# Kernel tuning notes

Hardware: AMD Instinct MI355X
Metric: run time of the kernel (lower is better)

## Reference

```python
import jax, jax.numpy as jnp
import numpy as np

T, B, I, H, O, L = 512, 64, 256, 1024, 256, 3


def _gru_layer(x_seq, h0, w_ih, w_hh, b_ih, b_hh):
    """PyTorch-style GRU layer. x_seq: [T,B,Iin], h0: [B,H].
    Gate order in stacked weights is (r, z, n), matching torch.nn.GRU."""
    # Precompute all input-side gate projections with one big GEMM: [T,B,3H]
    gi = jnp.einsum('tbi,gi->tbg', x_seq, w_ih) + b_ih

    def step(h, gi_t):
        gh = h @ w_hh.T + b_hh                      # [B,3H]
        i_r, i_z, i_n = jnp.split(gi_t, 3, axis=-1)
        h_r, h_z, h_n = jnp.split(gh, 3, axis=-1)
        r = jax.nn.sigmoid(i_r + h_r)
        z = jax.nn.sigmoid(i_z + h_z)
        n = jnp.tanh(i_n + r * h_n)
        h_new = (1.0 - z) * n + z * h
        return h_new, h_new

    h_last, ys = jax.lax.scan(step, h0, gi)
    return ys, h_last


def setup_inputs() -> dict:
    key = jax.random.key(0)
    ks = jax.random.split(key, 16)
    s = 1.0 / np.sqrt(H)  # torch init scale ~ U(-1/sqrt(H), 1/sqrt(H))
    inp = {
        'x': jax.random.normal(ks[0], (T, B, I), jnp.float32),
        'h0': jax.random.normal(ks[1], (L, B, H), jnp.float32),
        'fc_w': jax.random.uniform(ks[2], (O, H), jnp.float32, -s, s),
        'fc_b': jax.random.uniform(ks[3], (O,), jnp.float32, -s, s),
    }
    k_idx = 4
    for l in range(L):
        iin = I if l == 0 else H
        inp[f'w_ih_l{l}'] = jax.random.uniform(ks[k_idx], (3 * H, iin), jnp.float32, -s, s)
        inp[f'w_hh_l{l}'] = jax.random.uniform(ks[k_idx + 1], (3 * H, H), jnp.float32, -s, s)
        inp[f'b_ih_l{l}'] = jax.random.uniform(ks[k_idx + 2], (3 * H,), jnp.float32, -s, s)
        inp[f'b_hh_l{l}'] = jax.random.uniform(ks[k_idx + 3], (3 * H,), jnp.float32, -s, s)
        k_idx += 4
    return inp


def reference(x, h0,
              w_ih_l0, w_hh_l0, b_ih_l0, b_hh_l0,
              w_ih_l1, w_hh_l1, b_ih_l1, b_hh_l1,
              w_ih_l2, w_hh_l2, b_ih_l2, b_hh_l2,
              fc_w, fc_b):
    layer_params = [
        (w_ih_l0, w_hh_l0, b_ih_l0, b_hh_l0),
        (w_ih_l1, w_hh_l1, b_ih_l1, b_hh_l1),
        (w_ih_l2, w_hh_l2, b_ih_l2, b_hh_l2),
    ]
    out = x
    h_lasts = []
    for l, (wi, wh, bi, bh) in enumerate(layer_params):
        out, h_l = _gru_layer(out, h0[l], wi, wh, bi, bh)
        h_lasts.append(h_l)
    y = out @ fc_w.T + fc_b        # [T,B,O]
    h_final = jnp.stack(h_lasts)   # [L,B,H]
    return y, h_final
```

## Files before the change

### kernel.cpp

```cpp
#include <hip/hip_runtime.h>
#include <cstdint>
#include <cstddef>

#define TT 512
#define BB 64
#define II 256
#define HH 1024
#define OO 256
#define LL 3
#define NBLK 192
#define TSLOTS 513
#define DD 2
#define SSTEPS (TT + 2*DD + 1)
#define LDS_GI   98304
#define GI_STRIDE 68
#define LDS_HT   (98304 + 26112)
#define LDS_TOTAL (LDS_HT + 2048)

typedef _Float16 half8 __attribute__((ext_vector_type(8)));
typedef float floatx4 __attribute__((ext_vector_type(4)));
typedef float float4v __attribute__((ext_vector_type(4)));

__device__ __forceinline__ floatx4 mfma16(half8 a, half8 b, floatx4 c) {
    return __builtin_amdgcn_mfma_f32_16x16x32_f16(a, b, c, 0, 0, 0);
}

__device__ __forceinline__ half8 ld_f32x8_cvt(const float* p) {
    float4v a = *(const float4v*)p;
    float4v b = *(const float4v*)(p + 4);
    half8 v;
    v[0]=(_Float16)a[0]; v[1]=(_Float16)a[1]; v[2]=(_Float16)a[2]; v[3]=(_Float16)a[3];
    v[4]=(_Float16)b[0]; v[5]=(_Float16)b[1]; v[6]=(_Float16)b[2]; v[7]=(_Float16)b[3];
    return v;
}

__global__ void cast_f32_f16(const float* __restrict__ in, _Float16* __restrict__ out, int n) {
    int i = blockIdx.x * 256 + threadIdx.x;
    if (i < n) out[i] = (_Float16)in[i];
}

__global__ void init_h(const float* __restrict__ h0, float* __restrict__ h32,
                       _Float16* __restrict__ hseq, unsigned* __restrict__ bararea) {
    int i = blockIdx.x * 256 + threadIdx.x;
    if (i < 256) bararea[i] = 0u;
    if (i >= LL * BB * HH) return;
    int l = i / (BB * HH);
    int rest = i - l * (BB * HH);
    float v = h0[i];
    h32[((size_t)l * 2 + 0) * BB * HH + rest] = v;
    h32[((size_t)l * 2 + 1) * BB * HH + rest] = v;
    hseq[((size_t)l * TSLOTS) * BB * HH + rest] = (_Float16)v;
}

__global__ void frag_reorder(const float* __restrict__ src, _Float16* __restrict__ dst,
                             int K, int nks) {
    int idx = blockIdx.x * 256 + threadIdx.x;
    int total = 64 * 3 * nks * 64;
    if (idx >= total) return;
    int lane = idx & 63;
    int r = idx >> 6;
    int ks = r % nks; r /= nks;
    int g = r % 3;
    int jb = r / 3;
    int row = g * HH + jb * 16 + (lane & 15);
    int col = ks * 32 + (lane >> 4) * 8;
    const float* s8 = src + (size_t)row * K + col;
    half8 v;
#pragma unroll
    for (int i = 0; i < 8; ++i) v[i] = (_Float16)s8[i];
    *(half8*)(dst + (size_t)idx * 8) = v;
}

struct PArgs {
    const float* x;
    const _Float16* wih[3];
    const float* whh_src[3];
    const float* bih[3];
    const float* bhh[3];
    _Float16* hseq;
    float* h32;
    float* out_h;
    unsigned* flags;
    unsigned* rel;
};

__global__ __launch_bounds__(512, 2) void gru_persistent(PArgs a) {
    extern __shared__ __align__(16) char lds[];
    float* giL = (float*)(lds + LDS_GI);
    _Float16* ht = (_Float16*)(lds + LDS_HT);
    const int layer = blockIdx.x >> 6;
    const int jb = blockIdx.x & 63;
    const int tid = threadIdx.x;
    const int lane = tid & 63;
    const int wv = tid >> 6;
    const bool isrec = wv < 4;
    const int lr = lane & 15, lq = lane >> 4;
    const int row0 = (wv & 3) << 4;
    const int j = (jb << 4) + lr;

    const int wih_nks = (layer == 0) ? 8 : 32;
    const _Float16* wih = a.wih[layer] + (size_t)jb * (size_t)(3 * wih_nks * 64 * 8)
                          + (size_t)lane * 8;

    {
        const float* wsrc = a.whh_src[layer];
        for (int c = tid; c < 6144; c += 512) {
            int lc = c & 63;
            int ks = (c >> 6) & 31;
            int g  = c >> 11;
            int row = g * HH + (jb << 4) + (lc & 15);
            int col = (ks << 5) + ((lc >> 4) << 3);
            const float* s8 = wsrc + (size_t)row * HH + col;
            half8 v;
#pragma unroll
            for (int i = 0; i < 8; ++i) v[i] = (_Float16)s8[i];
            *(half8*)(lds + (size_t)c * 16) = v;
        }
    }
    __syncthreads();

    const float bir = a.bih[layer][j], biz = a.bih[layer][HH + j], bin = a.bih[layer][2 * HH + j];
    const float bhr = a.bhh[layer][j], bhz = a.bhh[layer][HH + j], bhn = a.bhh[layer][2 * HH + j];
    const char* wb = lds + (size_t)lane * 16;

    for (int s = 0; s < SSTEPS; ++s) {
        const int t = s - (2 * layer + 1);
        const int tp = s - 2 * layer;
        const bool rec_act = (t >= 0 && t < TT);
        const bool gi_act = (tp >= 0 && tp < TT);
        const int pr = (s + 1) & 1, pw = s & 1;

        if (isrec && rec_act) {
            floatx4 ar{0.f,0.f,0.f,0.f}, az{0.f,0.f,0.f,0.f}, anh{0.f,0.f,0.f,0.f};
            const _Float16* Ah = a.hseq + ((size_t)layer * TSLOTS + t) * BB * HH
                                 + (size_t)(row0 + lr) * HH + lq * 8;
#pragma unroll
            for (int ks = 0; ks < 32; ++ks) {
                half8 av = *(const half8*)(Ah + ks * 32);
                ar  = mfma16(av, *(const half8*)(wb + (0 * 32 + ks) * 1024), ar);
                az  = mfma16(av, *(const half8*)(wb + (1 * 32 + ks) * 1024), az);
                anh = mfma16(av, *(const half8*)(wb + (2 * 32 + ks) * 1024), anh);
            }
            const float* h32o = a.h32 + ((size_t)(layer * 2 + pr)) * BB * HH;
            float* h32n = a.h32 + ((size_t)(layer * 2 + pw)) * BB * HH;
#pragma unroll
            for (int i2 = 0; i2 < 4; ++i2) {
                int brow = row0 + lq * 4 + i2;
                float gir = giL[((pr * 3 + 0) * 16 + lr) * GI_STRIDE + brow];
                float giz = giL[((pr * 3 + 1) * 16 + lr) * GI_STRIDE + brow];
                float gin = giL[((pr * 3 + 2) * 16 + lr) * GI_STRIDE + brow];
                float rg = 1.f / (1.f + expf(-(ar[i2] + gir + bir + bhr)));
                float zg = 1.f / (1.f + expf(-(az[i2] + giz + biz + bhz)));
                float ng = tanhf(gin + bin + rg * (anh[i2] + bhn));
                float hold = h32o[(size_t)brow * HH + j];
                float hnew = (1.f - zg) * ng + zg * hold;
                h32n[(size_t)brow * HH + j] = hnew;
                ht[brow * 16 + lr] = (_Float16)hnew;
                if (t == TT - 1) a.out_h[((size_t)layer * BB + brow) * HH + j] = hnew;
            }
        }
        if (!isrec && gi_act) {
            floatx4 g0{0.f,0.f,0.f,0.f}, g1{0.f,0.f,0.f,0.f}, g2{0.f,0.f,0.f,0.f};
            if (layer == 0) {
                const float* Ax = a.x + (size_t)tp * BB * II + (size_t)(row0 + lr) * II + lq * 8;
#pragma unroll
                for (int ks = 0; ks < 8; ++ks) {
                    half8 av = ld_f32x8_cvt(Ax + ks * 32);
                    g0 = mfma16(av, *(const half8*)(wih + (size_t)(0 * 8 + ks) * 512), g0);
                    g1 = mfma16(av, *(const half8*)(wih + (size_t)(1 * 8 + ks) * 512), g1);
                    g2 = mfma16(av, *(const half8*)(wih + (size_t)(2 * 8 + ks) * 512), g2);
                }
            } else {
                const _Float16* Ay = a.hseq + ((size_t)(layer - 1) * TSLOTS + (tp + 1)) * BB * HH
                                     + (size_t)(row0 + lr) * HH + lq * 8;
#pragma unroll
                for (int ks = 0; ks < 32; ++ks) {
                    half8 av = *(const half8*)(Ay + ks * 32);
                    g0 = mfma16(av, *(const half8*)(wih + (size_t)(0 * 32 + ks) * 512), g0);
                    g1 = mfma16(av, *(const half8*)(wih + (size_t)(1 * 32 + ks) * 512), g1);
                    g2 = mfma16(av, *(const half8*)(wih + (size_t)(2 * 32 + ks) * 512), g2);
                }
            }
#pragma unroll
            for (int q = 0; q < 4; ++q) {
                int brow = row0 + lq * 4 + q;
                giL[((pw * 3 + 0) * 16 + lr) * GI_STRIDE + brow] = g0[q];
                giL[((pw * 3 + 1) * 16 + lr) * GI_STRIDE + brow] = g1[q];
                giL[((pw * 3 + 2) * 16 + lr) * GI_STRIDE + brow] = g2[q];
            }
        }
        __syncthreads();

        if (rec_act && tid < 256) {
            int row = tid >> 2, cg = tid & 3;
            unsigned long long v = *(const unsigned long long*)(ht + row * 16 + cg * 4);
            _Float16* dst = a.hseq + ((size_t)layer * TSLOTS + (t + 1)) * BB * HH
                            + (size_t)row * HH + (jb << 4) + cg * 4;
            __hip_atomic_store((unsigned long long*)dst, v,
                               __ATOMIC_RELAXED, __HIP_MEMORY_SCOPE_AGENT);
        }

        __syncthreads();
        if (tid == 0)
            __hip_atomic_store(&a.flags[blockIdx.x], (unsigned)(s + 1),
                               __ATOMIC_RELAXED, __HIP_MEMORY_SCOPE_AGENT);
        if (blockIdx.x == 0 && tid < 64) {
            const unsigned need = (unsigned)(s + 1);
            for (;;) {
                bool ok = true;
                for (int i = (int)tid; i < NBLK; i += 64)
                    ok = ok && (__hip_atomic_load(&a.flags[i], __ATOMIC_RELAXED,
                                                  __HIP_MEMORY_SCOPE_AGENT) >= need);
                if (__all(ok)) break;
                __builtin_amdgcn_s_sleep(1);
            }
            if (tid == 0)
                __hip_atomic_store(a.rel, need, __ATOMIC_RELAXED, __HIP_MEMORY_SCOPE_AGENT);
        }
        if (tid == 0) {
            while (__hip_atomic_load(a.rel, __ATOMIC_RELAXED,
                                     __HIP_MEMORY_SCOPE_AGENT) < (unsigned)(s + 1))
                __builtin_amdgcn_s_sleep(1);
        }
        __syncthreads();
        __builtin_amdgcn_sched_barrier(0);
    }
}

__global__ __launch_bounds__(256) void fc_kernel(const _Float16* __restrict__ hseq,
                                                 const _Float16* __restrict__ w,
                                                 const float* __restrict__ bias,
                                                 float* __restrict__ out) {
    const int wid = (blockIdx.x << 2) + (threadIdx.x >> 6);
    const int lane = threadIdx.x & 63;
    const int mt = wid >> 1;
    const int no = (wid & 1) * 8;
    const int lr = lane & 15, lq = lane >> 4;
    const _Float16* Ar = hseq + ((size_t)2 * TSLOTS * BB + BB + (size_t)(mt * 16 + lr)) * HH
                         + lq * 8;
    floatx4 acc[8] = {};
    for (int k = 0; k < HH; k += 32) {
        half8 av = *(const half8*)(Ar + k);
#pragma unroll
        for (int i = 0; i < 8; ++i) {
            const _Float16* Br = w + (size_t)((no + i) * 16 + lr) * HH + lq * 8 + k;
            acc[i] = mfma16(av, *(const half8*)Br, acc[i]);
        }
    }
#pragma unroll
    for (int i = 0; i < 8; ++i) {
        float b = bias[(no + i) * 16 + lr];
#pragma unroll
        for (int q = 0; q < 4; ++q)
            out[(size_t)(mt * 16 + lq * 4 + q) * OO + (no + i) * 16 + lr] = acc[i][q] + b;
    }
}

extern "C" void kernel_launch(void* const* d_in, const int* in_sizes, int n_in,
                              void* d_out, int out_size, void* d_ws, size_t ws_size,
                              hipStream_t stream) {
    const float* x    = (const float*)d_in[0];
    const float* h0   = (const float*)d_in[1];
    const float* fc_w = (const float*)d_in[2];
    const float* fc_b = (const float*)d_in[3];
    const float* wih[3]; const float* whh[3]; const float* bih[3]; const float* bhh[3];
    for (int l = 0; l < 3; ++l) {
        wih[l] = (const float*)d_in[4 + l * 4 + 0];
        whh[l] = (const float*)d_in[4 + l * 4 + 1];
        bih[l] = (const float*)d_in[4 + l * 4 + 2];
        bhh[l] = (const float*)d_in[4 + l * 4 + 3];
    }

    char* p = (char*)d_ws;
    auto alloc = [&](size_t bytes) {
        char* q = p;
        p += (bytes + 255) & ~(size_t)255;
        return q;
    };
    _Float16* hseq = (_Float16*)alloc((size_t)LL * TSLOTS * BB * HH * 2);
    _Float16* wihf[3];
    wihf[0] = (_Float16*)alloc((size_t)3 * HH * II * 2);
    wihf[1] = (_Float16*)alloc((size_t)3 * HH * HH * 2);
    wihf[2] = (_Float16*)alloc((size_t)3 * HH * HH * 2);
    _Float16* fcw16 = (_Float16*)alloc((size_t)OO * HH * 2);
    float* h32 = (float*)alloc((size_t)LL * 2 * BB * HH * 4);
    unsigned* bararea = (unsigned*)alloc(1024);
    if ((size_t)(p - (char*)d_ws) > ws_size) return;

    cast_f32_f16<<<(OO * HH + 255) / 256, 256, 0, stream>>>(fc_w, fcw16, OO * HH);
    frag_reorder<<<384, 256, 0, stream>>>(wih[0], wihf[0], II, 8);
    frag_reorder<<<1536, 256, 0, stream>>>(wih[1], wihf[1], HH, 32);
    frag_reorder<<<1536, 256, 0, stream>>>(wih[2], wihf[2], HH, 32);
    init_h<<<768, 256, 0, stream>>>(h0, h32, hseq, bararea);

    PArgs a;
    a.x = x;
    for (int l = 0; l < 3; ++l) {
        a.wih[l] = wihf[l];
        a.whh_src[l] = whh[l];
        a.bih[l] = bih[l];
        a.bhh[l] = bhh[l];
    }
    a.hseq = hseq; a.h32 = h32;
    a.out_h = (float*)d_out + (size_t)TT * BB * OO;
    a.flags = bararea;
    a.rel = bararea + 224;

    hipFuncSetAttribute((const void*)gru_persistent,
                        hipFuncAttributeMaxDynamicSharedMemorySize, LDS_TOTAL);
    gru_persistent<<<NBLK, 512, LDS_TOTAL, stream>>>(a);

    fc_kernel<<<1024, 256, 0, stream>>>(hseq, fcw16, fc_b, (float*)d_out);
}
```

Baseline: 8.684 ms.

## Replace global grid barrier with per-layer flag waits and keep hidden state in registers

Drops the centralized grid-wide barrier, where block 0 polled every flag and then released all blocks. Recurrent waves now spin only on their own layer's 64 flags, and input-projection waves spin on the previous layer's flags, so layers sync point-to-point. The fp32 previous hidden state moves from a global double buffer into registers, and sigmoid and tanh use hardware exp2 and reciprocal approximations. Together these cut per-step sync latency and global memory traffic, at the cost of lower-precision activations and a more delicate memory-ordering argument that relies on relaxed atomics.

New measurement: 10.09 ms. 1.16x slower.

```diff
diff --git a/kernel.cpp b/kernel.cpp
--- a/kernel.cpp
+++ b/kernel.cpp
@@ -10,11 +10,10 @@
 #define LL 3
 #define NBLK 192
 #define TSLOTS 513
-#define DD 2
-#define SSTEPS (TT + 2*DD + 1)
+#define SSTEPS (TT + 5)
 #define LDS_GI   98304
 #define GI_STRIDE 68
-#define LDS_HT   (98304 + 26112)
+#define LDS_HT   (LDS_GI + 26112)
 #define LDS_TOTAL (LDS_HT + 2048)
 
 typedef _Float16 half8 __attribute__((ext_vector_type(8)));
@@ -23,6 +22,13 @@
 
 __device__ __forceinline__ floatx4 mfma16(half8 a, half8 b, floatx4 c) {
     return __builtin_amdgcn_mfma_f32_16x16x32_f16(a, b, c, 0, 0, 0);
+}
+
+__device__ __forceinline__ float fast_sig(float x) {
+    return __builtin_amdgcn_rcpf(1.f + __builtin_amdgcn_exp2f(-1.44269504f * x));
+}
+__device__ __forceinline__ float fast_tanh(float x) {
+    return 1.f - 2.f * __builtin_amdgcn_rcpf(1.f + __builtin_amdgcn_exp2f(2.88539008f * x));
 }
 
 __device__ __forceinline__ half8 ld_f32x8_cvt(const float* p) {
@@ -39,17 +45,14 @@
     if (i < n) out[i] = (_Float16)in[i];
 }
 
-__global__ void init_h(const float* __restrict__ h0, float* __restrict__ h32,
-                       _Float16* __restrict__ hseq, unsigned* __restrict__ bararea) {
+__global__ void init_h(const float* __restrict__ h0, _Float16* __restrict__ hseq,
+                       unsigned* __restrict__ flags) {
     int i = blockIdx.x * 256 + threadIdx.x;
-    if (i < 256) bararea[i] = 0u;
+    if (i < 256) flags[i] = 0u;
     if (i >= LL * BB * HH) return;
     int l = i / (BB * HH);
     int rest = i - l * (BB * HH);
-    float v = h0[i];
-    h32[((size_t)l * 2 + 0) * BB * HH + rest] = v;
-    h32[((size_t)l * 2 + 1) * BB * HH + rest] = v;
-    hseq[((size_t)l * TSLOTS) * BB * HH + rest] = (_Float16)v;
+    hseq[((size_t)l * TSLOTS) * BB * HH + rest] = (_Float16)h0[i];
 }
 
 __global__ void frag_reorder(const float* __restrict__ src, _Float16* __restrict__ dst,
@@ -73,15 +76,14 @@
 
 struct PArgs {
     const float* x;
+    const float* h0;
     const _Float16* wih[3];
     const float* whh_src[3];
     const float* bih[3];
     const float* bhh[3];
     _Float16* hseq;
-    float* h32;
     float* out_h;
     unsigned* flags;
-    unsigned* rel;
 };
 
 __global__ __launch_bounds__(512, 2) void gru_persistent(PArgs a) {
@@ -123,14 +125,29 @@
     const float bhr = a.bhh[layer][j], bhz = a.bhh[layer][HH + j], bhn = a.bhh[layer][2 * HH + j];
     const char* wb = lds + (size_t)lane * 16;
 
+    float hprev[4];
+    if (isrec) {
+#pragma unroll
+        for (int i2 = 0; i2 < 4; ++i2)
+            hprev[i2] = a.h0[((size_t)layer * BB + row0 + lq * 4 + i2) * HH + j];
+    }
+
     for (int s = 0; s < SSTEPS; ++s) {
         const int t = s - (2 * layer + 1);
         const int tp = s - 2 * layer;
-        const bool rec_act = (t >= 0 && t < TT);
-        const bool gi_act = (tp >= 0 && tp < TT);
+        const bool rec_act = isrec && t >= 0 && t < TT;
+        const bool gi_act = !isrec && tp >= 0 && tp < TT;
         const int pr = (s + 1) & 1, pw = s & 1;
 
-        if (isrec && rec_act) {
+        if (rec_act) {
+            for (;;) {
+                unsigned f = __hip_atomic_load(&a.flags[layer * 64 + lane],
+                                               __ATOMIC_RELAXED, __HIP_MEMORY_SCOPE_AGENT);
+                if (__all(f >= (unsigned)s)) break;
+                __builtin_amdgcn_s_sleep(1);
+            }
+            __builtin_amdgcn_sched_barrier(0);
+
             floatx4 ar{0.f,0.f,0.f,0.f}, az{0.f,0.f,0.f,0.f}, anh{0.f,0.f,0.f,0.f};
             const _Float16* Ah = a.hseq + ((size_t)layer * TSLOTS + t) * BB * HH
                                  + (size_t)(row0 + lr) * HH + lq * 8;
@@ -141,25 +158,31 @@
                 az  = mfma16(av, *(const half8*)(wb + (1 * 32 + ks) * 1024), az);
                 anh = mfma16(av, *(const half8*)(wb + (2 * 32 + ks) * 1024), anh);
             }
-            const float* h32o = a.h32 + ((size_t)(layer * 2 + pr)) * BB * HH;
-            float* h32n = a.h32 + ((size_t)(layer * 2 + pw)) * BB * HH;
 #pragma unroll
             for (int i2 = 0; i2 < 4; ++i2) {
                 int brow = row0 + lq * 4 + i2;
                 float gir = giL[((pr * 3 + 0) * 16 + lr) * GI_STRIDE + brow];
                 float giz = giL[((pr * 3 + 1) * 16 + lr) * GI_STRIDE + brow];
                 float gin = giL[((pr * 3 + 2) * 16 + lr) * GI_STRIDE + brow];
-                float rg = 1.f / (1.f + expf(-(ar[i2] + gir + bir + bhr)));
-                float zg = 1.f / (1.f + expf(-(az[i2] + giz + biz + bhz)));
-                float ng = tanhf(gin + bin + rg * (anh[i2] + bhn));
-                float hold = h32o[(size_t)brow * HH + j];
-                float hnew = (1.f - zg) * ng + zg * hold;
-                h32n[(size_t)brow * HH + j] = hnew;
+                float rg = fast_sig(ar[i2] + gir + bir + bhr);
+                float zg = fast_sig(az[i2] + giz + biz + bhz);
+                float ng = fast_tanh(gin + bin + rg * (anh[i2] + bhn));
+                float hnew = (1.f - zg) * ng + zg * hprev[i2];
+                hprev[i2] = hnew;
                 ht[brow * 16 + lr] = (_Float16)hnew;
                 if (t == TT - 1) a.out_h[((size_t)layer * BB + brow) * HH + j] = hnew;
             }
         }
-        if (!isrec && gi_act) {
+        if (gi_act) {
+            if (layer > 0) {
+                for (;;) {
+                    unsigned f = __hip_atomic_load(&a.flags[(layer - 1) * 64 + lane],
+                                                   __ATOMIC_RELAXED, __HIP_MEMORY_SCOPE_AGENT);
+                    if (__all(f >= (unsigned)s)) break;
+                    __builtin_amdgcn_s_sleep(1);
+                }
+                __builtin_amdgcn_sched_barrier(0);
+            }
             floatx4 g0{0.f,0.f,0.f,0.f}, g1{0.f,0.f,0.f,0.f}, g2{0.f,0.f,0.f,0.f};
             if (layer == 0) {
                 const float* Ax = a.x + (size_t)tp * BB * II + (size_t)(row0 + lr) * II + lq * 8;
@@ -191,7 +214,7 @@
         }
         __syncthreads();
 
-        if (rec_act && tid < 256) {
+        if (rec_act) {
             int row = tid >> 2, cg = tid & 3;
             unsigned long long v = *(const unsigned long long*)(ht + row * 16 + cg * 4);
             _Float16* dst = a.hseq + ((size_t)layer * TSLOTS + (t + 1)) * BB * HH
@@ -199,31 +222,10 @@
             __hip_atomic_store((unsigned long long*)dst, v,
                                __ATOMIC_RELAXED, __HIP_MEMORY_SCOPE_AGENT);
         }
-
         __syncthreads();
         if (tid == 0)
             __hip_atomic_store(&a.flags[blockIdx.x], (unsigned)(s + 1),
                                __ATOMIC_RELAXED, __HIP_MEMORY_SCOPE_AGENT);
-        if (blockIdx.x == 0 && tid < 64) {
-            const unsigned need = (unsigned)(s + 1);
-            for (;;) {
-                bool ok = true;
-                for (int i = (int)tid; i < NBLK; i += 64)
-                    ok = ok && (__hip_atomic_load(&a.flags[i], __ATOMIC_RELAXED,
-                                                  __HIP_MEMORY_SCOPE_AGENT) >= need);
-                if (__all(ok)) break;
-                __builtin_amdgcn_s_sleep(1);
-            }
-            if (tid == 0)
-                __hip_atomic_store(a.rel, need, __ATOMIC_RELAXED, __HIP_MEMORY_SCOPE_AGENT);
-        }
-        if (tid == 0) {
-            while (__hip_atomic_load(a.rel, __ATOMIC_RELAXED,
-                                     __HIP_MEMORY_SCOPE_AGENT) < (unsigned)(s + 1))
-                __builtin_amdgcn_s_sleep(1);
-        }
-        __syncthreads();
-        __builtin_amdgcn_sched_barrier(0);
     }
 }
 
@@ -283,28 +285,27 @@
     wihf[1] = (_Float16*)alloc((size_t)3 * HH * HH * 2);
     wihf[2] = (_Float16*)alloc((size_t)3 * HH * HH * 2);
     _Float16* fcw16 = (_Float16*)alloc((size_t)OO * HH * 2);
-    float* h32 = (float*)alloc((size_t)LL * 2 * BB * HH * 4);
-    unsigned* bararea = (unsigned*)alloc(1024);
+    unsigned* flags = (unsigned*)alloc(1024);
     if ((size_t)(p - (char*)d_ws) > ws_size) return;
 
     cast_f32_f16<<<(OO * HH + 255) / 256, 256, 0, stream>>>(fc_w, fcw16, OO * HH);
     frag_reorder<<<384, 256, 0, stream>>>(wih[0], wihf[0], II, 8);
     frag_reorder<<<1536, 256, 0, stream>>>(wih[1], wihf[1], HH, 32);
     frag_reorder<<<1536, 256, 0, stream>>>(wih[2], wihf[2], HH, 32);
-    init_h<<<768, 256, 0, stream>>>(h0, h32, hseq, bararea);
+    init_h<<<768, 256, 0, stream>>>(h0, hseq, flags);
 
     PArgs a;
     a.x = x;
+    a.h0 = h0;
     for (int l = 0; l < 3; ++l) {
         a.wih[l] = wihf[l];
         a.whh_src[l] = whh[l];
         a.bih[l] = bih[l];
         a.bhh[l] = bhh[l];
     }
-    a.hseq = hseq; a.h32 = h32;
+    a.hseq = hseq;
     a.out_h = (float*)d_out + (size_t)TT * BB * OO;
-    a.flags = bararea;
-    a.rel = bararea + 224;
+    a.flags = flags;
 
     hipFuncSetAttribute((const void*)gru_persistent,
                         hipFuncAttributeMaxDynamicSharedMemorySize, LDS_TOTAL);
```
